# Kernel optimization log

Hardware: AMD Instinct MI355X
Metric: run time of the kernel (lower is better)

## Reference

```python
import jax, jax.numpy as jnp
import numpy as np

N, E, D, G, S, H = 100000, 1600000, 64, 1024, 4096, 128
BN_EPS = 1e-5


def setup_inputs() -> dict:
    key = jax.random.key(0)
    ks = jax.random.split(key, 24)
    x = jax.random.normal(ks[0], (N, D), jnp.float32)
    sid = jax.random.randint(ks[1], (N,), 0, S)
    x = x.at[:, 5].set(sid.astype(jnp.float32))  # column 5 holds integer substructure ids
    edge_index = jax.random.randint(ks[2], (2, E), 0, N, dtype=jnp.int32)
    batch = jnp.sort(jax.random.randint(ks[3], (N,), 0, G, dtype=jnp.int32))

    def lin(k, fan_in, shape):
        return jax.random.normal(k, shape, jnp.float32) / np.sqrt(fan_in)

    return {
        "x": x, "edge_index": edge_index, "batch": batch,
        # substructure attention net: Linear(D,64) -> tanh -> Linear(64,1,no bias)
        "w1": lin(ks[4], D, (D, 64)), "b1": jnp.zeros((64,), jnp.float32),
        "w2": lin(ks[5], 64, (64,)),
        "cw0": lin(ks[6], D + 1, (D + 1, H)), "cb0": jnp.zeros((H,), jnp.float32),
        "cw_rest": lin(ks[7], H, (3, H, H)), "cb_rest": jnp.zeros((3, H), jnp.float32),
        # BatchNorm1d (eval mode: running stats)
        "bn_gamma": jnp.ones((4, H), jnp.float32), "bn_beta": jnp.zeros((4, H), jnp.float32),
        "bn_mean": 0.1 * jax.random.normal(ks[8], (4, H), jnp.float32),
        "bn_var": jax.random.uniform(ks[9], (4, H), jnp.float32, 0.5, 1.5),
        # pred head: Linear(128,64) -> ELU -> Linear(64,1)
        "hw1": lin(ks[10], H, (H, 64)), "hb1": jnp.zeros((64,), jnp.float32),
        "hw2": lin(ks[11], 64, (64, 1)), "hb2": jnp.zeros((1,), jnp.float32),
    }


def _subst_attention(x, subst_ids, w1, b1, w2):
    ones = jnp.ones((x.shape[0],), x.dtype)
    cnt = jax.ops.segment_sum(ones, subst_ids, num_segments=S)
    sums = jax.ops.segment_sum(x, subst_ids, num_segments=S)
    means = sums / jnp.maximum(cnt, 1.0)[:, None]          # [S, D] per-substructure mean
    scores = jnp.tanh(means @ w1 + b1) @ w2                # [S]
    attn = jax.nn.softmax(scores, axis=0)                  # softmax over substructures
    return attn[subst_ids][:, None]                        # [N, 1] broadcast back to atoms


def _gcn(x, W, b, row, col, norm, n):
    h = x @ W                                              # [N, H]
    msg = h[row] * norm[:, None]                           # gather + scale  [E+N, H]
    return jax.ops.segment_sum(msg, col, num_segments=n) + b


def reference(x, edge_index, batch, w1, b1, w2, cw0, cb0, cw_rest, cb_rest,
              bn_gamma, bn_beta, bn_mean, bn_var, hw1, hb1, hw2, hb2):
    n = x.shape[0]
    subst_ids = jax.lax.stop_gradient(x[:, 5]).astype(jnp.int32)
    attn = _subst_attention(x, subst_ids, w1, b1, w2)
    h = jnp.concatenate([x, attn], axis=1)                 # [N, D+1]

    # add self loops, symmetric GCN normalization (as in PyG GCNConv)
    loops = jnp.arange(n, dtype=edge_index.dtype)
    row = jnp.concatenate([edge_index[0], loops])
    col = jnp.concatenate([edge_index[1], loops])
    deg = jax.ops.segment_sum(jnp.ones_like(row, dtype=h.dtype), col, num_segments=n)
    dinv = jax.lax.rsqrt(jnp.maximum(deg, 1.0))
    norm = dinv[row] * dinv[col]

    def bn(z, i):
        return (z - bn_mean[i]) * jax.lax.rsqrt(bn_var[i] + BN_EPS) * bn_gamma[i] + bn_beta[i]

    h = jax.nn.elu(bn(_gcn(h, cw0, cb0, row, col, norm, n), 0))
    for i in range(3):
        z = bn(_gcn(h, cw_rest[i], cb_rest[i], row, col, norm, n), i + 1)
        h = jax.nn.elu(z) if i < 2 else jax.nn.relu(z)

    # global mean pool over graphs
    gcnt = jax.ops.segment_sum(jnp.ones((n,), h.dtype), batch, num_segments=G)
    pooled = jax.ops.segment_sum(h, batch, num_segments=G) / jnp.maximum(gcnt, 1.0)[:, None]

    return jax.nn.elu(pooled @ hw1 + hb1) @ hw2 + hb2      # [G, 1]
```

## Files before the change

### kernel.cpp

```cpp
#include <hip/hip_runtime.h>
#include <math.h>

static constexpr int SS = 4096;
static constexpr int HH = 128;
static constexpr float EPS_BN = 1e-5f;

typedef __attribute__((ext_vector_type(8))) short bf16x8;
typedef __attribute__((ext_vector_type(4))) float f32x4;

__device__ inline unsigned short f2bf(float f) {
  unsigned int u = __float_as_uint(f);
  return (unsigned short)((u + 0x7fffu + ((u >> 16) & 1u)) >> 16);
}
__device__ inline float bflo(unsigned int u) { return __uint_as_float(u << 16); }
__device__ inline float bfhi(unsigned int u) { return __uint_as_float(u & 0xffff0000u); }


__global__ void gcn_subst_accum(const float* __restrict__ x, float* __restrict__ cnt,
                                float* __restrict__ sums, int n) {
  int node = blockIdx.x * 4 + (threadIdx.x >> 6);
  int lane = threadIdx.x & 63;
  if (node >= n) return;
  const float* xr = x + (size_t)node * 64;
  float v = xr[lane];
  int sid = (int)__shfl(v, 5, 64);
  if (lane == 0) atomicAdd(&cnt[sid], 1.0f);
  atomicAdd(&sums[(size_t)sid * 64 + lane], v);
}

__global__ void gcn_scores(const float* __restrict__ sums, const float* __restrict__ cnt,
                           const float* __restrict__ w1, const float* __restrict__ b1,
                           const float* __restrict__ w2, float* __restrict__ scores) {
  int s = blockIdx.x * 4 + (threadIdx.x >> 6);
  int j = threadIdx.x & 63;
  float r = 1.0f / fmaxf(cnt[s], 1.0f);
  const float* ss = sums + (size_t)s * 64;
  float acc = b1[j];
  #pragma unroll 8
  for (int d = 0; d < 64; ++d) acc = fmaf(ss[d] * r, w1[d * 64 + j], acc);
  float t = tanhf(acc) * w2[j];
  #pragma unroll
  for (int off = 32; off; off >>= 1) t += __shfl_down(t, off, 64);
  if (j == 0) scores[s] = t;
}

__global__ void gcn_softmax(float* __restrict__ sc) {
  int t = threadIdx.x;
  int wid = t >> 6;
  float v[4]; float m = -INFINITY;
  for (int i = 0; i < 4; ++i) { v[i] = sc[t + i * 1024]; m = fmaxf(m, v[i]); }
  for (int off = 32; off; off >>= 1) m = fmaxf(m, __shfl_xor(m, off, 64));
  __shared__ float wmax[16];
  if ((t & 63) == 0) wmax[wid] = m;
  __syncthreads();
  if (t == 0) { float mm = wmax[0]; for (int i = 1; i < 16; ++i) mm = fmaxf(mm, wmax[i]); wmax[0] = mm; }
  __syncthreads();
  float M = wmax[0];
  float s = 0.f;
  for (int i = 0; i < 4; ++i) { v[i] = expf(v[i] - M); s += v[i]; }
  for (int off = 32; off; off >>= 1) s += __shfl_xor(s, off, 64);
  __shared__ float wsum[16];
  if ((t & 63) == 0) wsum[wid] = s;
  __syncthreads();
  if (t == 0) { float ts = 0.f; for (int i = 0; i < 16; ++i) ts += wsum[i]; wsum[0] = ts; }
  __syncthreads();
  float inv = 1.0f / wsum[0];
  for (int i = 0; i < 4; ++i) sc[t + i * 1024] = v[i] * inv;
}


__global__ void gcn_pos(const int* __restrict__ col, int* __restrict__ fill,
                        int* __restrict__ pos, int e) {
  int i = blockIdx.x * 256 + threadIdx.x;
  if (i < e) pos[i] = atomicAdd(&fill[col[i]], 1);
}

__global__ void gcn_dinv(const int* __restrict__ fill, float* __restrict__ dinv, int n) {
  int i = blockIdx.x * 256 + threadIdx.x;
  if (i < n) dinv[i] = rsqrtf((float)fill[i] + 1.0f);
}

__global__ void gcn_scan1(const int* __restrict__ fill, int* __restrict__ rowstart,
                          int* __restrict__ bsum, int n) {
  __shared__ int tmp[1024];
  int t = threadIdx.x; int g = blockIdx.x * 1024 + t;
  int v = (g < n) ? fill[g] : 0;
  tmp[t] = v; __syncthreads();
  for (int off = 1; off < 1024; off <<= 1) {
    int a = (t >= off) ? tmp[t - off] : 0; __syncthreads();
    tmp[t] += a; __syncthreads();
  }
  if (g < n) rowstart[g] = tmp[t] - v;
  if (t == 1023) bsum[blockIdx.x] = tmp[t];
}

__global__ void gcn_scan2(int* __restrict__ bsum, int nb) {
  __shared__ int tmp[128];
  int t = threadIdx.x;
  int v = (t < nb) ? bsum[t] : 0;
  tmp[t] = v; __syncthreads();
  for (int off = 1; off < 128; off <<= 1) {
    int a = (t >= off) ? tmp[t - off] : 0; __syncthreads();
    tmp[t] += a; __syncthreads();
  }
  if (t < nb) bsum[t] = tmp[t] - v;
}

__global__ void gcn_scan3(int* __restrict__ rowstart, const int* __restrict__ bsum, int n, int e) {
  int g = blockIdx.x * 1024 + threadIdx.x;
  if (g < n) rowstart[g] += bsum[blockIdx.x];
  if (g == 0) rowstart[n] = e;
}

__global__ void gcn_scatter2(const int* __restrict__ row, const int* __restrict__ col,
                             const int* __restrict__ pos, const int* __restrict__ rowstart,
                             const float* __restrict__ dinv, int2* __restrict__ sedge, int e) {
  int i = blockIdx.x * 256 + threadIdx.x;
  if (i >= e) return;
  int c = col[i], r = row[i];
  sedge[rowstart[c] + pos[i]] = make_int2(r, __float_as_int(dinv[r] * dinv[c]));
}


__global__ void gcn_xb(const float* __restrict__ x, unsigned int* __restrict__ xh, int n) {
  int i = blockIdx.x * 256 + threadIdx.x;
  if (i >= n * 32) return;
  int pr = i & 31;
  float2 v = *(const float2*)&x[(size_t)(i >> 5) * 64 + pr * 2];
  if (pr == 2) v.y = 0.f;
  xh[i] = (unsigned int)f2bf(v.x) | ((unsigned int)f2bf(v.y) << 16);
}

__global__ void gcn_np(const float* __restrict__ x, const float* __restrict__ attn,
                       float2* __restrict__ np, int n) {
  int i = blockIdx.x * 256 + threadIdx.x;
  if (i >= n) return;
  int sid = (int)x[(size_t)i * 64 + 5];
  np[i] = make_float2((float)sid, attn[sid]);
}

__global__ void gcn_wpack(const float* __restrict__ W, unsigned short* __restrict__ out, int nkc) {
  int idx = blockIdx.x * 256 + threadIdx.x;
  if (idx >= 8 * nkc * 64) return;
  int lane = idx & 63;
  int kc = (idx >> 6) % nkc;
  int nt = idx / (64 * nkc);
  int colc = nt * 16 + (lane & 15);
  int k0 = kc * 32 + (lane >> 4) * 8;
  unsigned int w[4];
  #pragma unroll
  for (int i = 0; i < 4; ++i) {
    unsigned short a = f2bf(W[(size_t)(k0 + 2 * i) * 128 + colc]);
    unsigned short b = f2bf(W[(size_t)(k0 + 2 * i + 1) * 128 + colc]);
    w[i] = (unsigned int)a | ((unsigned int)b << 16);
  }
  *(uint4*)&out[(size_t)idx * 8] = make_uint4(w[0], w[1], w[2], w[3]);
}

__global__ void gcn_bnp(const float* __restrict__ cb0, const float* __restrict__ cbr,
                        const float* __restrict__ bng, const float* __restrict__ bnb,
                        const float* __restrict__ bnm, const float* __restrict__ bnv,
                        float* __restrict__ bnS, float* __restrict__ bnT) {
  int i = blockIdx.x * 128 + threadIdx.x;
  int l = i >> 7, c = i & 127;
  float S = rsqrtf(bnv[i] + EPS_BN) * bng[i];
  float bias = (l == 0) ? cb0[c] : cbr[(l - 1) * 128 + c];
  bnS[i] = S;
  bnT[i] = fmaf(bias - bnm[i], S, bnb[i]);
}


__global__ void gcn_agg_x(const unsigned int* __restrict__ xh, const int2* __restrict__ sedge,
                          const int* __restrict__ rowstart, const float* __restrict__ dinv,
                          unsigned int* __restrict__ s0b, int n) {
  int node = blockIdx.x * 4 + (threadIdx.x >> 6);
  int lane = threadIdx.x & 63;
  if (node >= n) return;
  float di = dinv[node], d2 = di * di;
  unsigned int us = xh[(size_t)node * 32 + (lane & 31)];
  float ax = (lane < 32) ? bflo(us) * d2 : 0.f;
  float ay = (lane < 32) ? bfhi(us) * d2 : 0.f;
  int s_ = rowstart[node], e_ = rowstart[node + 1];
  for (int b = s_; b < e_; b += 8) {
    int idx = b + (lane & 7);
    int2 se = (idx < e_) ? sedge[idx] : make_int2(node, 0);
    #pragma unroll
    for (int j = 0; j < 8; j += 2) {
      int sa = __shfl(se.x, j, 8), sb = __shfl(se.x, j + 1, 8);
      float wa = __int_as_float(__shfl(se.y, j, 8));
      float wb = __int_as_float(__shfl(se.y, j + 1, 8));
      int src = (lane < 32) ? sa : sb;
      float w = (lane < 32) ? wa : wb;
      unsigned int u = xh[(size_t)src * 32 + (lane & 31)];
      ax = fmaf(bflo(u), w, ax);
      ay = fmaf(bfhi(u), w, ay);
    }
  }
  ax += __shfl_xor(ax, 32, 64);
  ay += __shfl_xor(ay, 32, 64);
  if (lane < 32)
    s0b[(size_t)node * 32 + lane] = (unsigned int)f2bf(ax) | ((unsigned int)f2bf(ay) << 16);
}

__global__ void gcn_agg_np(const float2* __restrict__ np, const int2* __restrict__ sedge,
                           const int* __restrict__ rowstart, const float* __restrict__ dinv,
                           float* __restrict__ s0x, int n) {
  int i = blockIdx.x * 256 + threadIdx.x;
  if (i >= n) return;
  float di = dinv[i], d2 = di * di;
  float2 self = np[i];
  float a5 = d2 * self.x, a64 = d2 * self.y;
  int s_ = rowstart[i], e_ = rowstart[i + 1];
  for (int ee = s_; ee < e_; ++ee) {
    int2 se = sedge[ee];
    float w = __int_as_float(se.y);
    float2 v = np[se.x];
    a5 = fmaf(v.x, w, a5);
    a64 = fmaf(v.y, w, a64);
  }
  s0x[(size_t)i * 2] = a5;
  s0x[(size_t)i * 2 + 1] = a64;
}


__global__ void gcn_aggB(const unsigned short* __restrict__ hB, const int2* __restrict__ sedge,
                         const int* __restrict__ rowstart, const float* __restrict__ dinv,
                         unsigned int* __restrict__ sBb, int n) {
  int node = blockIdx.x * 4 + (threadIdx.x >> 6);
  int lane = threadIdx.x & 63;
  if (node >= n) return;
  float di = dinv[node], d2 = di * di;
  const unsigned int* h32 = (const unsigned int*)hB;
  unsigned int us = h32[(size_t)node * 64 + lane];
  float ax = bflo(us) * d2, ay = bfhi(us) * d2;
  int s_ = rowstart[node], e_ = rowstart[node + 1];
  for (int b = s_; b < e_; b += 8) {
    int idx = b + (lane & 7);
    int2 se = (idx < e_) ? sedge[idx] : make_int2(node, 0);
    #pragma unroll
    for (int j = 0; j < 8; ++j) {
      int src = __shfl(se.x, j, 8);
      float w = __int_as_float(__shfl(se.y, j, 8));
      unsigned int u = h32[(size_t)src * 64 + lane];
      ax = fmaf(bflo(u), w, ax);
      ay = fmaf(bfhi(u), w, ay);
    }
  }
  sBb[(size_t)node * 64 + lane] = (unsigned int)f2bf(ax) | ((unsigned int)f2bf(ay) << 16);
}


__global__ __launch_bounds__(256)
void gcn_mm_mfma(const unsigned short* __restrict__ A, const unsigned short* __restrict__ Wpk,
                 const float* __restrict__ bnS, const float* __restrict__ bnT,
                 unsigned short* __restrict__ hB, int relu) {
  __shared__ unsigned short tile[4][16][136];
  int t = threadIdx.x;
  int wid = t >> 6, l = t & 63;
  int rowA = l & 15, kg = l >> 4;
  size_t row0w = (size_t)blockIdx.x * 64 + wid * 16;
  const unsigned short* Ar = A + (row0w + rowA) * 128 + kg * 8;
  bf16x8 af[4];
  #pragma unroll
  for (int kc = 0; kc < 4; ++kc) af[kc] = *(const bf16x8*)(Ar + kc * 32);
  f32x4 acc[8];
  #pragma unroll
  for (int nt = 0; nt < 8; ++nt) acc[nt] = (f32x4){0.f, 0.f, 0.f, 0.f};
  const unsigned short* wp = Wpk + (size_t)l * 8;
  #pragma unroll
  for (int kc = 0; kc < 4; ++kc) {
    bf16x8 bf[8];
    #pragma unroll
    for (int nt = 0; nt < 8; ++nt)
      bf[nt] = *(const bf16x8*)(wp + (size_t)(nt * 4 + kc) * 512);
    #pragma unroll
    for (int nt = 0; nt < 8; ++nt)
      acc[nt] = __builtin_amdgcn_mfma_f32_16x16x32_bf16(af[kc], bf[nt], acc[nt], 0, 0, 0);
  }
  int colb = l & 15, rb = kg * 4;
  #pragma unroll
  for (int nt = 0; nt < 8; ++nt) {
    int c = nt * 16 + colb;
    float S = bnS[c], T = bnT[c];
    #pragma unroll
    for (int j = 0; j < 4; ++j) {
      float v = fmaf(acc[nt][j], S, T);
      v = relu ? fmaxf(v, 0.f) : (v > 0.f ? v : expf(v) - 1.f);
      tile[wid][rb + j][c] = f2bf(v);
    }
  }
  __syncthreads();
  #pragma unroll
  for (int i = 0; i < 4; ++i) {
    int m = i * 64 + l;
    int row = m >> 4, chunk = m & 15;
    uint4 v = *(const uint4*)&tile[wid][row][chunk * 8];
    *(uint4*)&hB[(row0w + row) * 128 + chunk * 8] = v;
  }
}

__global__ __launch_bounds__(256)
void gcn_mm0_mfma(const unsigned short* __restrict__ A, const float* __restrict__ s0x,
                  const unsigned short* __restrict__ Wpk0, const float* __restrict__ cw0,
                  const float* __restrict__ bnS, const float* __restrict__ bnT,
                  unsigned short* __restrict__ hB) {
  __shared__ unsigned short tile[4][16][136];
  int t = threadIdx.x;
  int wid = t >> 6, l = t & 63;
  int rowA = l & 15, kg = l >> 4;
  size_t row0w = (size_t)blockIdx.x * 64 + wid * 16;
  const unsigned short* Ar = A + (row0w + rowA) * 64 + kg * 8;
  bf16x8 af[2];
  #pragma unroll
  for (int kc = 0; kc < 2; ++kc) af[kc] = *(const bf16x8*)(Ar + kc * 32);
  f32x4 acc[8];
  #pragma unroll
  for (int nt = 0; nt < 8; ++nt) acc[nt] = (f32x4){0.f, 0.f, 0.f, 0.f};
  const unsigned short* wp = Wpk0 + (size_t)l * 8;
  #pragma unroll
  for (int kc = 0; kc < 2; ++kc) {
    bf16x8 bf[8];
    #pragma unroll
    for (int nt = 0; nt < 8; ++nt)
      bf[nt] = *(const bf16x8*)(wp + (size_t)(nt * 2 + kc) * 512);
    #pragma unroll
    for (int nt = 0; nt < 8; ++nt)
      acc[nt] = __builtin_amdgcn_mfma_f32_16x16x32_bf16(af[kc], bf[nt], acc[nt], 0, 0, 0);
  }
  int colb = l & 15, rb = kg * 4;
  float2 ax[4];
  #pragma unroll
  for (int j = 0; j < 4; ++j) ax[j] = *(const float2*)&s0x[(row0w + rb + j) * 2];
  #pragma unroll
  for (int nt = 0; nt < 8; ++nt) {
    int c = nt * 16 + colb;
    float w5 = cw0[5 * 128 + c], w64 = cw0[64 * 128 + c];
    float S = bnS[c], T = bnT[c];
    #pragma unroll
    for (int j = 0; j < 4; ++j) {
      float z = acc[nt][j] + ax[j].x * w5 + ax[j].y * w64;
      float v = fmaf(z, S, T);
      v = v > 0.f ? v : expf(v) - 1.f;
      tile[wid][rb + j][c] = f2bf(v);
    }
  }
  __syncthreads();
  #pragma unroll
  for (int i = 0; i < 4; ++i) {
    int m = i * 64 + l;
    int row = m >> 4, chunk = m & 15;
    uint4 v = *(const uint4*)&tile[wid][row][chunk * 8];
    *(uint4*)&hB[(row0w + row) * 128 + chunk * 8] = v;
  }
}


__global__ void gcn_gb(const int* __restrict__ batch, int* __restrict__ gstart, int n, int G) {
  int g = blockIdx.x * 256 + threadIdx.x;
  if (g > G) return;
  if (g == G) { gstart[G] = n; return; }
  int lo = 0, hi = n;
  while (lo < hi) { int mid = (lo + hi) >> 1; if (batch[mid] < g) lo = mid + 1; else hi = mid; }
  gstart[g] = lo;
}

__global__ void gcn_pool2(const unsigned short* __restrict__ hB, const int* __restrict__ gstart,
                          float* __restrict__ pooled, int G) {
  int g = blockIdx.x * 4 + (threadIdx.x >> 6);
  int lane = threadIdx.x & 63;
  if (g >= G) return;
  int s = gstart[g], epos = gstart[g + 1];
  const unsigned int* h32 = (const unsigned int*)hB;
  float ax = 0.f, ay = 0.f;
  for (int i = s; i < epos; ++i) {
    unsigned int u = h32[(size_t)i * 64 + lane];
    ax += bflo(u);
    ay += bfhi(u);
  }
  float r = 1.0f / fmaxf((float)(epos - s), 1.0f);
  ((float2*)pooled)[(size_t)g * 64 + lane] = make_float2(ax * r, ay * r);
}

__global__ void gcn_head(const float* __restrict__ pooled,
                         const float* __restrict__ hw1, const float* __restrict__ hb1,
                         const float* __restrict__ hw2, const float* __restrict__ hb2,
                         float* __restrict__ out, int g) {
  int gi = blockIdx.x * 4 + (threadIdx.x >> 6);
  int j = threadIdx.x & 63;
  if (gi >= g) return;
  const float* p = pooled + (size_t)gi * 128;
  float acc = hb1[j];
  #pragma unroll 8
  for (int k = 0; k < 128; ++k) acc = fmaf(p[k], hw1[k * 64 + j], acc);
  float t = acc > 0.f ? acc : expf(acc) - 1.f;
  t *= hw2[j];
  #pragma unroll
  for (int off = 32; off; off >>= 1) t += __shfl_down(t, off, 64);
  if (j == 0) out[gi] = t + hb2[0];
}


extern "C" void kernel_launch(void* const* d_in, const int* in_sizes, int n_in,
                              void* d_out, int out_size, void* d_ws, size_t ws_size,
                              hipStream_t stream) {
  const float* x   = (const float*)d_in[0];
  const int*   ei  = (const int*)d_in[1];
  const int*   batch = (const int*)d_in[2];
  const float* w1  = (const float*)d_in[3];
  const float* b1  = (const float*)d_in[4];
  const float* w2  = (const float*)d_in[5];
  const float* cw0 = (const float*)d_in[6];
  const float* cb0 = (const float*)d_in[7];
  const float* cwr = (const float*)d_in[8];
  const float* cbr = (const float*)d_in[9];
  const float* bng = (const float*)d_in[10];
  const float* bnb = (const float*)d_in[11];
  const float* bnm = (const float*)d_in[12];
  const float* bnv = (const float*)d_in[13];
  const float* hw1 = (const float*)d_in[14];
  const float* hb1 = (const float*)d_in[15];
  const float* hw2 = (const float*)d_in[16];
  const float* hb2 = (const float*)d_in[17];
  float* out = (float*)d_out;
  (void)n_in; (void)ws_size;

  const int n = in_sizes[0] / 64;
  const int e = in_sizes[1] / 2;
  const int G = out_size;
  const int* row = ei;
  const int* col = ei + e;
  const int nb128 = (n + 127) / 128;
  const int n_pad = nb128 * 128;

  char* p = (char*)d_ws;
  auto take = [&](size_t bytes) { char* r = p; p += (bytes + 255) & ~(size_t)255; return r; };
  float* cnt    = (float*)take((size_t)SS * 4);
  float* sums   = (float*)take((size_t)SS * 64 * 4);
  float* attn   = (float*)take((size_t)SS * 4);
  float* dinv   = (float*)take((size_t)n * 4);
  int*   rowst  = (int*)take(((size_t)n + 1) * 4);
  int*   fill   = (int*)take((size_t)n * 4);
  int*   pos    = (int*)take((size_t)e * 4);
  int*   bsum   = (int*)take(128 * 4);
  int*   gstart = (int*)take(((size_t)G + 1) * 4);
  int2*  sedge  = (int2*)take((size_t)e * 8);
  float* pooled = (float*)take((size_t)G * HH * 4);
  float2* np    = (float2*)take((size_t)n * 8);
  unsigned int* xh = (unsigned int*)take((size_t)n * 32 * 4);
  unsigned int* s0b = (unsigned int*)take((size_t)n_pad * 32 * 4);
  float* s0x    = (float*)take((size_t)n_pad * 2 * 4);
  unsigned int* sBb = (unsigned int*)take((size_t)n_pad * 64 * 4);
  unsigned short* hB = (unsigned short*)take((size_t)n_pad * HH * 2);
  unsigned short* wpk0 = (unsigned short*)take((size_t)8 * 2 * 64 * 8 * 2);
  unsigned short* wpkr = (unsigned short*)take((size_t)3 * 8 * 4 * 64 * 8 * 2);
  float* bnS    = (float*)take(4 * 128 * 4);
  float* bnT    = (float*)take(4 * 128 * 4);

  hipMemsetAsync(cnt, 0, (size_t)SS * 4, stream);
  hipMemsetAsync(sums, 0, (size_t)SS * 64 * 4, stream);
  hipMemsetAsync(fill, 0, (size_t)n * 4, stream);

  gcn_subst_accum<<<(n + 3) / 4, 256, 0, stream>>>(x, cnt, sums, n);
  gcn_scores<<<SS / 4, 256, 0, stream>>>(sums, cnt, w1, b1, w2, attn);
  gcn_softmax<<<1, 1024, 0, stream>>>(attn);

  gcn_pos<<<(e + 255) / 256, 256, 0, stream>>>(col, fill, pos, e);
  gcn_dinv<<<(n + 255) / 256, 256, 0, stream>>>(fill, dinv, n);
  int nb = (n + 1023) / 1024;
  gcn_scan1<<<nb, 1024, 0, stream>>>(fill, rowst, bsum, n);
  gcn_scan2<<<1, 128, 0, stream>>>(bsum, nb);
  gcn_scan3<<<nb, 1024, 0, stream>>>(rowst, bsum, n, e);
  gcn_scatter2<<<(e + 255) / 256, 256, 0, stream>>>(row, col, pos, rowst, dinv, sedge, e);
  gcn_gb<<<(G + 256) / 256, 256, 0, stream>>>(batch, gstart, n, G);

  gcn_xb<<<(n * 32 + 255) / 256, 256, 0, stream>>>(x, xh, n);
  gcn_np<<<(n + 255) / 256, 256, 0, stream>>>(x, attn, np, n);
  gcn_wpack<<<(8 * 2 * 64 + 255) / 256, 256, 0, stream>>>(cw0, wpk0, 2);
  for (int l = 0; l < 3; ++l)
    gcn_wpack<<<(8 * 4 * 64 + 255) / 256, 256, 0, stream>>>(cwr + (size_t)l * HH * HH,
        wpkr + (size_t)l * 8 * 4 * 64 * 8, 4);
  gcn_bnp<<<4, 128, 0, stream>>>(cb0, cbr, bng, bnb, bnm, bnv, bnS, bnT);

  gcn_agg_x<<<(n + 3) / 4, 256, 0, stream>>>(xh, sedge, rowst, dinv, s0b, n);
  gcn_agg_np<<<(n + 255) / 256, 256, 0, stream>>>(np, sedge, rowst, dinv, s0x, n);
  gcn_mm0_mfma<<<n_pad / 64, 256, 0, stream>>>((const unsigned short*)s0b, s0x, wpk0, cw0,
      bnS, bnT, hB);

  for (int l = 0; l < 3; ++l) {
    gcn_aggB<<<(n + 3) / 4, 256, 0, stream>>>(hB, sedge, rowst, dinv, sBb, n);
    gcn_mm_mfma<<<n_pad / 64, 256, 0, stream>>>((const unsigned short*)sBb,
        wpkr + (size_t)l * 8 * 4 * 64 * 8, bnS + (l + 1) * 128, bnT + (l + 1) * 128,
        hB, l == 2 ? 1 : 0);
  }

  gcn_pool2<<<(G + 3) / 4, 256, 0, stream>>>(hB, gstart, pooled, G);
  gcn_head<<<(G + 3) / 4, 256, 0, stream>>>(pooled, hw1, hb1, hw2, hb2, out, G);
}
```

Before: 647.7 us.

## Merge front-end kernels into multi-role launches and widen aggregation gathers

Folds many small preprocessing kernels (edge positions, substructure accumulation, bf16 conversion, graph starts, weight packing, BN params) into one block-partitioned launch. The dinv computation moves into the scan, and scatter/np and agg_x/agg_np are each merged into one launch. The aggregation kernels now gather neighbour rows with 16-byte loads, so several edges are processed per wavefront in parallel and then reduced with shuffles. This cuts launch count and per-edge load instructions, at the cost of extra register use and cross-lane reductions.

```diff
diff --git a/kernel.cpp b/kernel.cpp
--- a/kernel.cpp
+++ b/kernel.cpp
@@ -16,17 +16,96 @@
 __device__ inline float bfhi(unsigned int u) { return __uint_as_float(u & 0xffff0000u); }
 
 
-__global__ void gcn_subst_accum(const float* __restrict__ x, float* __restrict__ cnt,
-                                float* __restrict__ sums, int n) {
-  int node = blockIdx.x * 4 + (threadIdx.x >> 6);
-  int lane = threadIdx.x & 63;
-  if (node >= n) return;
-  const float* xr = x + (size_t)node * 64;
-  float v = xr[lane];
-  int sid = (int)__shfl(v, 5, 64);
-  if (lane == 0) atomicAdd(&cnt[sid], 1.0f);
-  atomicAdd(&sums[(size_t)sid * 64 + lane], v);
-}
+__device__ void wpack_body(const float* __restrict__ W, unsigned short* __restrict__ out,
+                           int nkc, int idx) {
+  if (idx >= 8 * nkc * 64) return;
+  int lane = idx & 63;
+  int kc = (idx >> 6) % nkc;
+  int nt = idx / (64 * nkc);
+  int colc = nt * 16 + (lane & 15);
+  int k0 = kc * 32 + (lane >> 4) * 8;
+  unsigned int w[4];
+  #pragma unroll
+  for (int i = 0; i < 4; ++i) {
+    unsigned short a = f2bf(W[(size_t)(k0 + 2 * i) * 128 + colc]);
+    unsigned short b = f2bf(W[(size_t)(k0 + 2 * i + 1) * 128 + colc]);
+    w[i] = (unsigned int)a | ((unsigned int)b << 16);
+  }
+  *(uint4*)&out[(size_t)idx * 8] = make_uint4(w[0], w[1], w[2], w[3]);
+}
+
+__global__ __launch_bounds__(256)
+void gcn_front1(const int* __restrict__ col, int* __restrict__ fill, int* __restrict__ pos,
+                const float* __restrict__ x, float* __restrict__ cnt, float* __restrict__ sums,
+                unsigned int* __restrict__ xh, const int* __restrict__ batch,
+                int* __restrict__ gstart,
+                const float* __restrict__ cw0, const float* __restrict__ cwr,
+                unsigned short* __restrict__ wpk0, unsigned short* __restrict__ wpkr,
+                const float* __restrict__ cb0, const float* __restrict__ cbr,
+                const float* __restrict__ bng, const float* __restrict__ bnb,
+                const float* __restrict__ bnm, const float* __restrict__ bnv,
+                float* __restrict__ bnS, float* __restrict__ bnT,
+                int n, int e, int G,
+                int nbPos, int nbSub, int nbXb, int nbGb, int nbW0, int nbWr) {
+  int b = blockIdx.x;
+  int t = threadIdx.x;
+  if (b < nbPos) {
+    int i = b * 256 + t;
+    if (i < e) pos[i] = atomicAdd(&fill[col[i]], 1);
+    return;
+  }
+  b -= nbPos;
+  if (b < nbSub) {
+    int node = b * 4 + (t >> 6);
+    int lane = t & 63;
+    if (node >= n) return;
+    const float* xr = x + (size_t)node * 64;
+    float v = xr[lane];
+    int sid = (int)__shfl(v, 5, 64);
+    if (lane == 0) atomicAdd(&cnt[sid], 1.0f);
+    atomicAdd(&sums[(size_t)sid * 64 + lane], v);
+    return;
+  }
+  b -= nbSub;
+  if (b < nbXb) {
+    int i = b * 256 + t;
+    if (i >= n * 32) return;
+    int pr = i & 31;
+    float2 v = *(const float2*)&x[(size_t)(i >> 5) * 64 + pr * 2];
+    if (pr == 2) v.y = 0.f;
+    xh[i] = (unsigned int)f2bf(v.x) | ((unsigned int)f2bf(v.y) << 16);
+    return;
+  }
+  b -= nbXb;
+  if (b < nbGb) {
+    int g = b * 256 + t;
+    if (g > G) return;
+    if (g == G) { gstart[G] = n; return; }
+    int lo = 0, hi = n;
+    while (lo < hi) { int mid = (lo + hi) >> 1; if (batch[mid] < g) lo = mid + 1; else hi = mid; }
+    gstart[g] = lo;
+    return;
+  }
+  b -= nbGb;
+  if (b < nbW0) { wpack_body(cw0, wpk0, 2, b * 256 + t); return; }
+  b -= nbW0;
+  if (b < 3 * nbWr) {
+    int l = b / nbWr, bb = b % nbWr;
+    wpack_body(cwr + (size_t)l * HH * HH, wpkr + (size_t)l * 8 * 4 * 64 * 8, 4, bb * 256 + t);
+    return;
+  }
+  b -= 3 * nbWr;
+  {
+    int i = b * 256 + t;
+    if (i >= 512) return;
+    int l = i >> 7, c = i & 127;
+    float S = rsqrtf(bnv[i] + EPS_BN) * bng[i];
+    float bias = (l == 0) ? cb0[c] : cbr[(l - 1) * 128 + c];
+    bnS[i] = S;
+    bnT[i] = fmaf(bias - bnm[i], S, bnb[i]);
+  }
+}
+
 
 __global__ void gcn_scores(const float* __restrict__ sums, const float* __restrict__ cnt,
                            const float* __restrict__ w1, const float* __restrict__ b1,
@@ -69,22 +148,12 @@
 }
 
 
-__global__ void gcn_pos(const int* __restrict__ col, int* __restrict__ fill,
-                        int* __restrict__ pos, int e) {
-  int i = blockIdx.x * 256 + threadIdx.x;
-  if (i < e) pos[i] = atomicAdd(&fill[col[i]], 1);
-}
-
-__global__ void gcn_dinv(const int* __restrict__ fill, float* __restrict__ dinv, int n) {
-  int i = blockIdx.x * 256 + threadIdx.x;
-  if (i < n) dinv[i] = rsqrtf((float)fill[i] + 1.0f);
-}
-
 __global__ void gcn_scan1(const int* __restrict__ fill, int* __restrict__ rowstart,
-                          int* __restrict__ bsum, int n) {
+                          int* __restrict__ bsum, float* __restrict__ dinv, int n) {
   __shared__ int tmp[1024];
   int t = threadIdx.x; int g = blockIdx.x * 1024 + t;
   int v = (g < n) ? fill[g] : 0;
+  if (g < n) dinv[g] = rsqrtf((float)v + 1.0f);
   tmp[t] = v; __syncthreads();
   for (int off = 1; off < 1024; off <<= 1) {
     int a = (t >= off) ? tmp[t - off] : 0; __syncthreads();
@@ -112,100 +181,86 @@
   if (g == 0) rowstart[n] = e;
 }
 
-__global__ void gcn_scatter2(const int* __restrict__ row, const int* __restrict__ col,
-                             const int* __restrict__ pos, const int* __restrict__ rowstart,
-                             const float* __restrict__ dinv, int2* __restrict__ sedge, int e) {
-  int i = blockIdx.x * 256 + threadIdx.x;
+
+__global__ __launch_bounds__(256)
+void gcn_front3(const float* __restrict__ x, const float* __restrict__ attn,
+                float2* __restrict__ np,
+                const int* __restrict__ row, const int* __restrict__ col,
+                const int* __restrict__ pos, const int* __restrict__ rowstart,
+                const float* __restrict__ dinv, int2* __restrict__ sedge,
+                int n, int e, int nbNp) {
+  int b = blockIdx.x;
+  int t = threadIdx.x;
+  if (b < nbNp) {
+    int i = b * 256 + t;
+    if (i >= n) return;
+    int sid = (int)x[(size_t)i * 64 + 5];
+    np[i] = make_float2((float)sid, attn[sid]);
+    return;
+  }
+  b -= nbNp;
+  int i = b * 256 + t;
   if (i >= e) return;
   int c = col[i], r = row[i];
   sedge[rowstart[c] + pos[i]] = make_int2(r, __float_as_int(dinv[r] * dinv[c]));
 }
 
 
-__global__ void gcn_xb(const float* __restrict__ x, unsigned int* __restrict__ xh, int n) {
-  int i = blockIdx.x * 256 + threadIdx.x;
-  if (i >= n * 32) return;
-  int pr = i & 31;
-  float2 v = *(const float2*)&x[(size_t)(i >> 5) * 64 + pr * 2];
-  if (pr == 2) v.y = 0.f;
-  xh[i] = (unsigned int)f2bf(v.x) | ((unsigned int)f2bf(v.y) << 16);
-}
-
-__global__ void gcn_np(const float* __restrict__ x, const float* __restrict__ attn,
-                       float2* __restrict__ np, int n) {
-  int i = blockIdx.x * 256 + threadIdx.x;
-  if (i >= n) return;
-  int sid = (int)x[(size_t)i * 64 + 5];
-  np[i] = make_float2((float)sid, attn[sid]);
-}
-
-__global__ void gcn_wpack(const float* __restrict__ W, unsigned short* __restrict__ out, int nkc) {
-  int idx = blockIdx.x * 256 + threadIdx.x;
-  if (idx >= 8 * nkc * 64) return;
-  int lane = idx & 63;
-  int kc = (idx >> 6) % nkc;
-  int nt = idx / (64 * nkc);
-  int colc = nt * 16 + (lane & 15);
-  int k0 = kc * 32 + (lane >> 4) * 8;
-  unsigned int w[4];
-  #pragma unroll
-  for (int i = 0; i < 4; ++i) {
-    unsigned short a = f2bf(W[(size_t)(k0 + 2 * i) * 128 + colc]);
-    unsigned short b = f2bf(W[(size_t)(k0 + 2 * i + 1) * 128 + colc]);
-    w[i] = (unsigned int)a | ((unsigned int)b << 16);
-  }
-  *(uint4*)&out[(size_t)idx * 8] = make_uint4(w[0], w[1], w[2], w[3]);
-}
-
-__global__ void gcn_bnp(const float* __restrict__ cb0, const float* __restrict__ cbr,
-                        const float* __restrict__ bng, const float* __restrict__ bnb,
-                        const float* __restrict__ bnm, const float* __restrict__ bnv,
-                        float* __restrict__ bnS, float* __restrict__ bnT) {
-  int i = blockIdx.x * 128 + threadIdx.x;
-  int l = i >> 7, c = i & 127;
-  float S = rsqrtf(bnv[i] + EPS_BN) * bng[i];
-  float bias = (l == 0) ? cb0[c] : cbr[(l - 1) * 128 + c];
-  bnS[i] = S;
-  bnT[i] = fmaf(bias - bnm[i], S, bnb[i]);
-}
-
-
-__global__ void gcn_agg_x(const unsigned int* __restrict__ xh, const int2* __restrict__ sedge,
-                          const int* __restrict__ rowstart, const float* __restrict__ dinv,
-                          unsigned int* __restrict__ s0b, int n) {
-  int node = blockIdx.x * 4 + (threadIdx.x >> 6);
-  int lane = threadIdx.x & 63;
-  if (node >= n) return;
-  float di = dinv[node], d2 = di * di;
-  unsigned int us = xh[(size_t)node * 32 + (lane & 31)];
-  float ax = (lane < 32) ? bflo(us) * d2 : 0.f;
-  float ay = (lane < 32) ? bfhi(us) * d2 : 0.f;
-  int s_ = rowstart[node], e_ = rowstart[node + 1];
-  for (int b = s_; b < e_; b += 8) {
-    int idx = b + (lane & 7);
-    int2 se = (idx < e_) ? sedge[idx] : make_int2(node, 0);
-    #pragma unroll
-    for (int j = 0; j < 8; j += 2) {
-      int sa = __shfl(se.x, j, 8), sb = __shfl(se.x, j + 1, 8);
-      float wa = __int_as_float(__shfl(se.y, j, 8));
-      float wb = __int_as_float(__shfl(se.y, j + 1, 8));
-      int src = (lane < 32) ? sa : sb;
-      float w = (lane < 32) ? wa : wb;
-      unsigned int u = xh[(size_t)src * 32 + (lane & 31)];
-      ax = fmaf(bflo(u), w, ax);
-      ay = fmaf(bfhi(u), w, ay);
-    }
-  }
-  ax += __shfl_xor(ax, 32, 64);
-  ay += __shfl_xor(ay, 32, 64);
-  if (lane < 32)
-    s0b[(size_t)node * 32 + lane] = (unsigned int)f2bf(ax) | ((unsigned int)f2bf(ay) << 16);
-}
-
-__global__ void gcn_agg_np(const float2* __restrict__ np, const int2* __restrict__ sedge,
-                           const int* __restrict__ rowstart, const float* __restrict__ dinv,
-                           float* __restrict__ s0x, int n) {
-  int i = blockIdx.x * 256 + threadIdx.x;
+__global__ __launch_bounds__(256)
+void gcn_front4(const unsigned int* __restrict__ xh, const float2* __restrict__ np,
+                const int2* __restrict__ sedge, const int* __restrict__ rowstart,
+                const float* __restrict__ dinv,
+                unsigned int* __restrict__ s0b, float* __restrict__ s0x,
+                int n, int nbAx) {
+  int blk = blockIdx.x;
+  int t = threadIdx.x;
+  if (blk < nbAx) {
+    int node = blk * 4 + (t >> 6);
+    int lane = t & 63;
+    if (node >= n) return;
+    int g = lane >> 3, sl = lane & 7;
+    float di = dinv[node], d2 = di * di;
+    const uint4* x4 = (const uint4*)xh;
+    float a[8];
+    if (g == 0) {
+      uint4 u = x4[(size_t)node * 8 + sl];
+      a[0] = bflo(u.x) * d2; a[1] = bfhi(u.x) * d2;
+      a[2] = bflo(u.y) * d2; a[3] = bfhi(u.y) * d2;
+      a[4] = bflo(u.z) * d2; a[5] = bfhi(u.z) * d2;
+      a[6] = bflo(u.w) * d2; a[7] = bfhi(u.w) * d2;
+    } else {
+      #pragma unroll
+      for (int i = 0; i < 8; ++i) a[i] = 0.f;
+    }
+    int s_ = rowstart[node], e_ = rowstart[node + 1];
+    for (int b = s_; b < e_; b += 8) {
+      int idx = b + (lane & 7);
+      int2 se = (idx < e_) ? sedge[idx] : make_int2(node, 0);
+      int src = __shfl(se.x, g, 8);
+      float w = __int_as_float(__shfl(se.y, g, 8));
+      uint4 u = x4[(size_t)src * 8 + sl];
+      a[0] = fmaf(bflo(u.x), w, a[0]); a[1] = fmaf(bfhi(u.x), w, a[1]);
+      a[2] = fmaf(bflo(u.y), w, a[2]); a[3] = fmaf(bfhi(u.y), w, a[3]);
+      a[4] = fmaf(bflo(u.z), w, a[4]); a[5] = fmaf(bfhi(u.z), w, a[5]);
+      a[6] = fmaf(bflo(u.w), w, a[6]); a[7] = fmaf(bfhi(u.w), w, a[7]);
+    }
+    #pragma unroll
+    for (int i = 0; i < 8; ++i) {
+      a[i] += __shfl_xor(a[i], 8, 64);
+      a[i] += __shfl_xor(a[i], 16, 64);
+      a[i] += __shfl_xor(a[i], 32, 64);
+    }
+    if (g == 0) {
+      uint4 o;
+      o.x = (unsigned)f2bf(a[0]) | ((unsigned)f2bf(a[1]) << 16);
+      o.y = (unsigned)f2bf(a[2]) | ((unsigned)f2bf(a[3]) << 16);
+      o.z = (unsigned)f2bf(a[4]) | ((unsigned)f2bf(a[5]) << 16);
+      o.w = (unsigned)f2bf(a[6]) | ((unsigned)f2bf(a[7]) << 16);
+      ((uint4*)s0b)[(size_t)node * 8 + sl] = o;
+    }
+    return;
+  }
+  int i = (blk - nbAx) * 256 + t;
   if (i >= n) return;
   float di = dinv[i], d2 = di * di;
   float2 self = np[i];
@@ -223,30 +278,55 @@
 }
 
 
-__global__ void gcn_aggB(const unsigned short* __restrict__ hB, const int2* __restrict__ sedge,
-                         const int* __restrict__ rowstart, const float* __restrict__ dinv,
-                         unsigned int* __restrict__ sBb, int n) {
+__global__ __launch_bounds__(256)
+void gcn_aggB(const unsigned short* __restrict__ hB, const int2* __restrict__ sedge,
+              const int* __restrict__ rowstart, const float* __restrict__ dinv,
+              unsigned int* __restrict__ sBb, int n) {
   int node = blockIdx.x * 4 + (threadIdx.x >> 6);
   int lane = threadIdx.x & 63;
   if (node >= n) return;
+  int g = lane >> 4, sl = lane & 15;
   float di = dinv[node], d2 = di * di;
-  const unsigned int* h32 = (const unsigned int*)hB;
-  unsigned int us = h32[(size_t)node * 64 + lane];
-  float ax = bflo(us) * d2, ay = bfhi(us) * d2;
+  const uint4* h4 = (const uint4*)hB;
+  float a[8];
+  if (g == 0) {
+    uint4 u = h4[(size_t)node * 16 + sl];
+    a[0] = bflo(u.x) * d2; a[1] = bfhi(u.x) * d2;
+    a[2] = bflo(u.y) * d2; a[3] = bfhi(u.y) * d2;
+    a[4] = bflo(u.z) * d2; a[5] = bfhi(u.z) * d2;
+    a[6] = bflo(u.w) * d2; a[7] = bfhi(u.w) * d2;
+  } else {
+    #pragma unroll
+    for (int i = 0; i < 8; ++i) a[i] = 0.f;
+  }
   int s_ = rowstart[node], e_ = rowstart[node + 1];
   for (int b = s_; b < e_; b += 8) {
     int idx = b + (lane & 7);
     int2 se = (idx < e_) ? sedge[idx] : make_int2(node, 0);
     #pragma unroll
-    for (int j = 0; j < 8; ++j) {
-      int src = __shfl(se.x, j, 8);
-      float w = __int_as_float(__shfl(se.y, j, 8));
-      unsigned int u = h32[(size_t)src * 64 + lane];
-      ax = fmaf(bflo(u), w, ax);
-      ay = fmaf(bfhi(u), w, ay);
-    }
-  }
-  sBb[(size_t)node * 64 + lane] = (unsigned int)f2bf(ax) | ((unsigned int)f2bf(ay) << 16);
+    for (int j = 0; j < 2; ++j) {
+      int src = __shfl(se.x, j * 4 + g, 8);
+      float w = __int_as_float(__shfl(se.y, j * 4 + g, 8));
+      uint4 u = h4[(size_t)src * 16 + sl];
+      a[0] = fmaf(bflo(u.x), w, a[0]); a[1] = fmaf(bfhi(u.x), w, a[1]);
+      a[2] = fmaf(bflo(u.y), w, a[2]); a[3] = fmaf(bfhi(u.y), w, a[3]);
+      a[4] = fmaf(bflo(u.z), w, a[4]); a[5] = fmaf(bfhi(u.z), w, a[5]);
+      a[6] = fmaf(bflo(u.w), w, a[6]); a[7] = fmaf(bfhi(u.w), w, a[7]);
+    }
+  }
+  #pragma unroll
+  for (int i = 0; i < 8; ++i) {
+    a[i] += __shfl_xor(a[i], 16, 64);
+    a[i] += __shfl_xor(a[i], 32, 64);
+  }
+  if (g == 0) {
+    uint4 o;
+    o.x = (unsigned)f2bf(a[0]) | ((unsigned)f2bf(a[1]) << 16);
+    o.y = (unsigned)f2bf(a[2]) | ((unsigned)f2bf(a[3]) << 16);
+    o.z = (unsigned)f2bf(a[4]) | ((unsigned)f2bf(a[5]) << 16);
+    o.w = (unsigned)f2bf(a[6]) | ((unsigned)f2bf(a[7]) << 16);
+    ((uint4*)sBb)[(size_t)node * 16 + sl] = o;
+  }
 }
 
 
@@ -354,15 +434,6 @@
   }
 }
 
-
-__global__ void gcn_gb(const int* __restrict__ batch, int* __restrict__ gstart, int n, int G) {
-  int g = blockIdx.x * 256 + threadIdx.x;
-  if (g > G) return;
-  if (g == G) { gstart[G] = n; return; }
-  int lo = 0, hi = n;
-  while (lo < hi) { int mid = (lo + hi) >> 1; if (batch[mid] < g) lo = mid + 1; else hi = mid; }
-  gstart[g] = lo;
-}
 
 __global__ void gcn_pool2(const unsigned short* __restrict__ hB, const int* __restrict__ gstart,
                           float* __restrict__ pooled, int G) {
@@ -460,29 +531,30 @@
   hipMemsetAsync(sums, 0, (size_t)SS * 64 * 4, stream);
   hipMemsetAsync(fill, 0, (size_t)n * 4, stream);
 
-  gcn_subst_accum<<<(n + 3) / 4, 256, 0, stream>>>(x, cnt, sums, n);
+  int nbPos = (e + 255) / 256;
+  int nbSub = (n + 3) / 4;
+  int nbXb  = (n * 32 + 255) / 256;
+  int nbGb  = (G + 1 + 255) / 256;
+  int nbW0 = 4, nbWr = 8, nbBnp = 2;
+  int front1 = nbPos + nbSub + nbXb + nbGb + nbW0 + 3 * nbWr + nbBnp;
+  gcn_front1<<<front1, 256, 0, stream>>>(col, fill, pos, x, cnt, sums, xh, batch, gstart,
+      cw0, cwr, wpk0, wpkr, cb0, cbr, bng, bnb, bnm, bnv, bnS, bnT,
+      n, e, G, nbPos, nbSub, nbXb, nbGb, nbW0, nbWr);
+
   gcn_scores<<<SS / 4, 256, 0, stream>>>(sums, cnt, w1, b1, w2, attn);
   gcn_softmax<<<1, 1024, 0, stream>>>(attn);
 
-  gcn_pos<<<(e + 255) / 256, 256, 0, stream>>>(col, fill, pos, e);
-  gcn_dinv<<<(n + 255) / 256, 256, 0, stream>>>(fill, dinv, n);
   int nb = (n + 1023) / 1024;
-  gcn_scan1<<<nb, 1024, 0, stream>>>(fill, rowst, bsum, n);
+  gcn_scan1<<<nb, 1024, 0, stream>>>(fill, rowst, bsum, dinv, n);
   gcn_scan2<<<1, 128, 0, stream>>>(bsum, nb);
   gcn_scan3<<<nb, 1024, 0, stream>>>(rowst, bsum, n, e);
-  gcn_scatter2<<<(e + 255) / 256, 256, 0, stream>>>(row, col, pos, rowst, dinv, sedge, e);
-  gcn_gb<<<(G + 256) / 256, 256, 0, stream>>>(batch, gstart, n, G);
-
-  gcn_xb<<<(n * 32 + 255) / 256, 256, 0, stream>>>(x, xh, n);
-  gcn_np<<<(n + 255) / 256, 256, 0, stream>>>(x, attn, np, n);
-  gcn_wpack<<<(8 * 2 * 64 + 255) / 256, 256, 0, stream>>>(cw0, wpk0, 2);
-  for (int l = 0; l < 3; ++l)
-    gcn_wpack<<<(8 * 4 * 64 + 255) / 256, 256, 0, stream>>>(cwr + (size_t)l * HH * HH,
-        wpkr + (size_t)l * 8 * 4 * 64 * 8, 4);
-  gcn_bnp<<<4, 128, 0, stream>>>(cb0, cbr, bng, bnb, bnm, bnv, bnS, bnT);
-
-  gcn_agg_x<<<(n + 3) / 4, 256, 0, stream>>>(xh, sedge, rowst, dinv, s0b, n);
-  gcn_agg_np<<<(n + 255) / 256, 256, 0, stream>>>(np, sedge, rowst, dinv, s0x, n);
+
+  int nbNp = (n + 255) / 256, nbSc = (e + 255) / 256;
+  gcn_front3<<<nbNp + nbSc, 256, 0, stream>>>(x, attn, np, row, col, pos, rowst, dinv,
+      sedge, n, e, nbNp);
+
+  int nbAx = (n + 3) / 4, nbAnp = (n + 255) / 256;
+  gcn_front4<<<nbAx + nbAnp, 256, 0, stream>>>(xh, np, sedge, rowst, dinv, s0b, s0x, n, nbAx);
   gcn_mm0_mfma<<<n_pad / 64, 256, 0, stream>>>((const unsigned short*)s0b, s0x, wpk0, cw0,
       bnS, bnT, hB);
 
```

New measurement: 634.6 us. 1.02x faster.
